# Kernel optimization log

Hardware: AMD Instinct MI355X
Metric: run time of the kernel (lower is better)

Reference implementation:

```python
import jax, jax.numpy as jnp
import numpy as np

UNITS = 1024
N_CLASSES = 41
SUBSAMPLE = 4
KERNEL = 3
FEAT = 256


def setup_inputs() -> dict:
    key = jax.random.key(0)
    ks = jax.random.split(key, 12)
    B, T, F, U, C = 32, 1000, FEAT, UNITS, N_CLASSES
    s = lambda k, shape, sc: jax.random.normal(k, shape, dtype=jnp.float32) * sc
    return {
        "x": jax.random.normal(ks[0], (B, T, F), dtype=jnp.float32),
        # depthwise conv kernel: (width, 1, channels) for WIO with groups=C
        "conv_w": s(ks[1], (KERNEL, 1, F), 0.1),
        "h0_init": s(ks[2], (1, U), 0.05),
        "w0_x": s(ks[3], (F, 3 * U), 1.0 / np.sqrt(F)),
        "w0_h": s(ks[4], (U, 3 * U), 1.0 / np.sqrt(U)),
        "b0": jnp.zeros((2, 3 * U), dtype=jnp.float32),
        "w1_x": s(ks[5], (U, 3 * U), 1.0 / np.sqrt(U)),
        "w1_h": s(ks[6], (U, 3 * U), 1.0 / np.sqrt(U)),
        "b1": jnp.zeros((2, 3 * U), dtype=jnp.float32),
        "dense_w": s(ks[7], (U, C), 1.0 / np.sqrt(U)),
        "dense_b": jnp.zeros((C,), dtype=jnp.float32),
    }


def _depthwise_conv1d(x, w):
    # x: [B, T, C], w: [K, 1, C]; SAME padding, groups = C, relu, no bias
    C = x.shape[-1]
    y = jax.lax.conv_general_dilated(
        x, w, window_strides=(1,), padding="SAME",
        dimension_numbers=("NWC", "WIO", "NWC"), feature_group_count=C)
    return jax.nn.relu(y)


def _gru_layer(x, h0, Wx, Wh, b):
    # Keras GRU v2 (reset_after=True), gate order z, r, h.
    # x: [B, T, F]; h0: [B, U]; Wx: [F, 3U]; Wh: [U, 3U]; b: [2, 3U]
    xproj = jnp.einsum("btf,fg->btg", x, Wx) + b[0]  # [B, T, 3U]
    br = b[1]

    def step(h, xp):
        rec = h @ Wh + br  # [B, 3U]
        xz, xr, xh = jnp.split(xp, 3, axis=-1)
        rz, rr, rh = jnp.split(rec, 3, axis=-1)
        z = jax.nn.sigmoid(xz + rz)
        r = jax.nn.sigmoid(xr + rr)
        hh = jnp.tanh(xh + r * rh)
        hn = z * h + (1.0 - z) * hh
        return hn, hn

    _, ys = jax.lax.scan(step, h0, jnp.swapaxes(xproj, 0, 1))  # [T, B, U]
    return jnp.swapaxes(ys, 0, 1)


def reference(x, conv_w, h0_init, w0_x, w0_h, b0, w1_x, w1_h, b1, dense_w, dense_b):
    B = x.shape[0]
    U = w0_h.shape[0]
    h = _depthwise_conv1d(x, conv_w)
    # layer 0: learned initial state tiled over batch
    h = _gru_layer(h, jnp.tile(h0_init, (B, 1)), w0_x, w0_h, b0)
    # subsample after layer nLayers-2 == 0
    h = h[:, ::SUBSAMPLE, :]
    # layer 1: zero initial state (Keras default when initial_state is None)
    h = _gru_layer(h, jnp.zeros((B, U), dtype=x.dtype), w1_x, w1_h, b1)
    return h @ dense_w + dense_b  # [B, T//4, nClasses]
```

## Files before the change

kernel.cpp:

```cpp
#include <hip/hip_runtime.h>

typedef unsigned int u32;
typedef unsigned long long u64;
typedef unsigned short u16;
typedef __attribute__((ext_vector_type(8))) short short8;
typedef __attribute__((ext_vector_type(4))) float f32x4;
typedef __attribute__((ext_vector_type(4))) unsigned int u32x4;

#define MFMA(a,b,c) __builtin_amdgcn_mfma_f32_16x16x32_bf16((a),(b),(c),0,0,0)
#define ALOAD32(p)    __hip_atomic_load((p), __ATOMIC_RELAXED, __HIP_MEMORY_SCOPE_AGENT)
#define ASTORE32(p,v) __hip_atomic_store((p),(v), __ATOMIC_RELAXED, __HIP_MEMORY_SCOPE_AGENT)

__device__ __forceinline__ float bf2f(u32 b){ union{u32 u; float f;} v; v.u = b<<16; return v.f; }
__device__ __forceinline__ u16 f2bf(float f){ union{float f; u32 u;} v; v.f = f; u32 u = v.u;
  return (u16)((u + 0x7fffu + ((u>>16)&1u)) >> 16); }
__device__ __forceinline__ u32 pack_f(float v){
  u16 hi = f2bf(v); u16 lo = f2bf(v - bf2f(hi)); return (u32)hi | ((u32)lo<<16); }

__device__ __forceinline__ void unpack8(uint4 a, uint4 b, short8& hi, short8& lo){
  u32 w[8] = {a.x,a.y,a.z,a.w,b.x,b.y,b.z,b.w};
#pragma unroll
  for (int j=0;j<8;++j){ hi[j] = (short)(w[j] & 0xffffu); lo[j] = (short)(w[j] >> 16); }
}
__device__ __forceinline__ void unpackh4(u32x4 a, short8& hi){
#pragma unroll
  for (int i=0;i<4;++i){ hi[2*i] = (short)(a[i] & 0xffffu); hi[2*i+1] = (short)(a[i] >> 16); }
}

constexpr size_t OFF_Y    = 0;
constexpr size_t OFF_SUB  = 32768000;
constexpr size_t OFF_W0XH = 65536000;
constexpr size_t OFF_W0XL = 67108864;
constexpr size_t OFF_W0HH = 68681728;
constexpr size_t OFF_W0HL = 74973184;
constexpr size_t OFF_W1XH = 81264640;
constexpr size_t OFF_W1XL = 87556096;
constexpr size_t OFF_W1HH = 93847552;
constexpr size_t OFF_W1HL = 100139008;
constexpr size_t OFF_HB0  = 106430464;
constexpr size_t OFF_HB1  = 106692608;
constexpr size_t OFF_FL0  = 106954752;
constexpr size_t OFF_FL1  = 106955776;
constexpr size_t WS_NEED  = 106956800;

__global__ void build_frags(const float* __restrict__ W, u16* __restrict__ fhi,
                            u16* __restrict__ flo, int K){
  const int KT = K >> 8;
  size_t total = (size_t)K * 12 * 256;
  for (size_t i = (size_t)blockIdx.x*blockDim.x + threadIdx.x; i < total;
       i += (size_t)gridDim.x*blockDim.x){
    int j = (int)(i & 7); size_t r = i >> 3;
    int c = (int)(r % 12); r /= 12;
    int kseg = (int)(r & 3); r >>= 2;
    int kt = (int)(r % KT); r /= KT;
    int kq = (int)(r & 7); r >>= 3;
    int wg = (int)r;
    int k = kq*(K>>3) + kt*32 + kseg*8 + j;
    int col = (c>>2)*1024 + wg*4 + (c&3);
    float v = W[(size_t)k*3072 + col];
    u16 hi = f2bf(v);
    u16 lo = f2bf(v - bf2f(hi));
    fhi[i] = hi; flo[i] = lo;
  }
}

__global__ void init_state(const float* __restrict__ h0, u32* hb0, u32* hb1,
                           int* f0, int* f1){
  int i = blockIdx.x*blockDim.x + threadIdx.x;
  if (i < 256){ f0[i]=0; f1[i]=0; }
  if (i < 16384){
    int p = i & 511;
    u32 v = (u32)f2bf(h0[2*p]) | ((u32)f2bf(h0[2*p+1]) << 16);
    hb0[i] = v;
    hb1[i] = 0u;
  }
}

__global__ void conv_pack(const float* __restrict__ x, const float* __restrict__ cw,
                          u32* __restrict__ yp){
  for (size_t i = (size_t)blockIdx.x*blockDim.x + threadIdx.x; i < 8192000ull;
       i += (size_t)gridDim.x*blockDim.x){
    int f = (int)(i & 255); int b = (int)((i>>8)&31); int t = (int)(i>>13);
    const float* xb = x + ((size_t)b*1000 + t)*256 + f;
    float acc = xb[0]*cw[256+f];
    if (t > 0)   acc += xb[-256]*cw[f];
    if (t < 999) acc += xb[256]*cw[512+f];
    acc = fmaxf(acc, 0.0f);
    yp[i] = pack_f(acc);
  }
}

template<int LAYER>
__global__ __launch_bounds__(1024, 1)
void gru_persist(const u32* __restrict__ xin,
                 const u16* __restrict__ wxf_hi, const u16* __restrict__ wxf_lo,
                 const u16* __restrict__ whf_hi, const u16* __restrict__ whf_lo,
                 const float* __restrict__ bias,
                 u32* hbuf, int* flags, u32* out_pack)
{
  constexpr int T   = (LAYER==0) ? 1000 : 250;
  constexpr int KX  = (LAYER==0) ? 256 : 1024;
  constexpr int KTX = KX >> 8;
  __shared__ u16 WxHi[8*KTX*512], WxLo[8*KTX*512];
  __shared__ u16 WhHi[8*4*512],  WhLo[8*4*512];
  __shared__ float exch[8*32*18];
  __shared__ float harr[128];
  __shared__ int hready[32];

  const int tid  = threadIdx.x;
  const int wg   = blockIdx.x;
  const int lane = tid & 63;
  const int wave = tid >> 6;
  const int m    = wave & 1;
  const int kq   = wave >> 1;
  const int u0   = wg * 4;
  const int lo16 = lane & 15, hi16 = lane >> 4;
  const int lane_off = hi16*128 + lo16*8;
  const int hsel = (kq >= 4) ? 16 : 0;

  {
    for (int i = tid; i < 8*KTX*512/4; i += 1024){ ((u64*)WxHi)[i]=0; ((u64*)WxLo)[i]=0; }
    for (int i = tid; i < 8*4*512/4;  i += 1024){ ((u64*)WhHi)[i]=0; ((u64*)WhLo)[i]=0; }
    if (tid < 32) hready[tid] = 0;
  }
  __syncthreads();
  {
    const u16* bx_hi = wxf_hi + (size_t)wg*KX*12;
    const u16* bx_lo = wxf_lo + (size_t)wg*KX*12;
    const u16* bh_hi = whf_hi + (size_t)wg*1024*12;
    const u16* bh_lo = whf_lo + (size_t)wg*1024*12;
    for (int i = tid; i < 8*KTX*48; i += 1024){
      int c = i % 12; int r = i/12; int kseg = r & 3; r >>= 2;
      int kt = r % KTX; int kqq = r / KTX;
      int ldsoff = ((kqq*KTX+kt)*4+kseg)*128 + c*8;
      *(short8*)&WxHi[ldsoff] = *(const short8*)&bx_hi[(size_t)i*8];
      *(short8*)&WxLo[ldsoff] = *(const short8*)&bx_lo[(size_t)i*8];
    }
    for (int i = tid; i < 8*4*48; i += 1024){
      int c = i % 12; int r = i/12; int kseg = r & 3; r >>= 2;
      int kt = r & 3; int kqq = r >> 2;
      int cm = (c < 8) ? c : (c + 4);
      int ldsoff = ((kqq*4+kt)*4+kseg)*128 + cm*8;
      *(short8*)&WhHi[ldsoff] = *(const short8*)&bh_hi[(size_t)i*8];
      *(short8*)&WhLo[ldsoff] = *(const short8*)&bh_lo[(size_t)i*8];
    }
    if (tid < 128){
      u16 hv = ((const u16*)hbuf)[(tid>>2)*1024 + u0 + (tid&3)];
      harr[tid] = bf2f((u32)hv);
    }
  }
  __syncthreads();

  const int eb = tid >> 2, eu_l = tid & 3, eu = u0 + eu_l;
  const float zb  = bias[eu]        + bias[3072 + eu];
  const float rbv = bias[1024 + eu] + bias[4096 + eu];
  const float hxb = bias[2048 + eu];
  const float hrb = bias[5120 + eu];

  for (int t = 0; t < T; ++t) {
    const int cur = t & 1, nxt = cur ^ 1;
    f32x4 xacc = (f32x4){0.f,0.f,0.f,0.f};
    f32x4 racc = (f32x4){0.f,0.f,0.f,0.f};
    {
      const u32* xrow = xin + ((size_t)t*32 + 16*m + lo16)*KX + kq*(KX>>3) + hi16*8;
#pragma unroll
      for (int kt = 0; kt < KTX; ++kt) {
        uint4 a0 = *(const uint4*)(xrow + kt*32);
        uint4 a1 = *(const uint4*)(xrow + kt*32 + 4);
        short8 ahi, alo; unpack8(a0, a1, ahi, alo);
        short8 bhi = *(const short8*)&WxHi[(kq*KTX+kt)*512 + lane_off];
        short8 blo = *(const short8*)&WxLo[(kq*KTX+kt)*512 + lane_off];
        xacc = MFMA(ahi, bhi, xacc);
        xacc = MFMA(alo, bhi, xacc);
        xacc = MFMA(ahi, blo, xacc);
      }
    }
    if (t > 0) {
      if (wave == 0) {
        int f0, f1;
        do { f0 = ALOAD32(flags + lane); f1 = ALOAD32(flags + 64 + lane); }
        while (!__all(f0 >= t && f1 >= t));
        asm volatile("" ::: "memory");
        if (lane == 0) ((volatile int*)hready)[0] = t;
      } else if (wave == 1) {
        int f2, f3;
        do { f2 = ALOAD32(flags + 128 + lane); f3 = ALOAD32(flags + 192 + lane); }
        while (!__all(f2 >= t && f3 >= t));
        asm volatile("" ::: "memory");
        if (lane == 0) ((volatile int*)hready)[16] = t;
      }
      while (((volatile int*)hready)[hsel] < t) { }
      asm volatile("" ::: "memory");
    }
    {
      const u32* hrow = hbuf + cur*16384 + (16*m + lo16)*512 + kq*64 + hi16*4;
      u32x4 qa, qb, qc, qd;
      asm volatile(
        "global_load_dwordx4 %0, %4, off sc0 sc1\n\t"
        "global_load_dwordx4 %1, %4, off offset:64 sc0 sc1\n\t"
        "global_load_dwordx4 %2, %4, off offset:128 sc0 sc1\n\t"
        "global_load_dwordx4 %3, %4, off offset:192 sc0 sc1\n\t"
        "s_waitcnt vmcnt(0)"
        : "=&v"(qa), "=&v"(qb), "=&v"(qc), "=&v"(qd)
        : "v"(hrow)
        : "memory");
      short8 ah0, ah1, ah2, ah3;
      unpackh4(qa, ah0); unpackh4(qb, ah1); unpackh4(qc, ah2); unpackh4(qd, ah3);
      {
        short8 bhi = *(const short8*)&WhHi[(kq*4+0)*512 + lane_off];
        short8 blo = *(const short8*)&WhLo[(kq*4+0)*512 + lane_off];
        racc = MFMA(ah0, bhi, racc); racc = MFMA(ah0, blo, racc);
      }
      {
        short8 bhi = *(const short8*)&WhHi[(kq*4+1)*512 + lane_off];
        short8 blo = *(const short8*)&WhLo[(kq*4+1)*512 + lane_off];
        racc = MFMA(ah1, bhi, racc); racc = MFMA(ah1, blo, racc);
      }
      {
        short8 bhi = *(const short8*)&WhHi[(kq*4+2)*512 + lane_off];
        short8 blo = *(const short8*)&WhLo[(kq*4+2)*512 + lane_off];
        racc = MFMA(ah2, bhi, racc); racc = MFMA(ah2, blo, racc);
      }
      {
        short8 bhi = *(const short8*)&WhHi[(kq*4+3)*512 + lane_off];
        short8 blo = *(const short8*)&WhLo[(kq*4+3)*512 + lane_off];
        racc = MFMA(ah3, bhi, racc); racc = MFMA(ah3, blo, racc);
      }
    }
    {
      const int bb = 16*m + hi16*4;
#pragma unroll
      for (int r4 = 0; r4 < 4; ++r4)
        exch[(kq*32 + bb + r4)*18 + lo16] = xacc[r4] + racc[r4];
    }
    __syncthreads();
    u32 pk_out = 0;
    if (tid < 128) {
      float zp=0.f, rp=0.f, xh=0.f, rh=0.f;
#pragma unroll
      for (int qd = 0; qd < 8; ++qd) {
        const float* e = &exch[(qd*32 + eb)*18];
        zp += e[eu_l];
        rp += e[4 + eu_l];
        xh += e[8 + eu_l];
        rh += e[12 + eu_l];
      }
      float z = 1.f/(1.f + __expf(-(zp + zb)));
      float r = 1.f/(1.f + __expf(-(rp + rbv)));
      float pre = xh + hxb + r*(rh + hrb);
      float ex = __expf(-2.f*fabsf(pre));
      float th = (1.f - ex)/(1.f + ex);
      float hh = copysignf(th, pre);
      float hn = z*harr[tid] + (1.f - z)*hh;
      harr[tid] = hn;
      pk_out = pack_f(hn);
      int pk16 = (int)(pk_out & 0xffffu);
      int prt  = __shfl_xor(pk16, 1);
      if ((tid & 1) == 0) {
        u32 pair = (u32)pk16 | ((u32)prt << 16);
        ASTORE32(hbuf + nxt*16384 + eb*512 + wg*2 + (eu_l>>1), pair);
      }
    }
    asm volatile("s_waitcnt vmcnt(0)" ::: "memory");
    __syncthreads();
    if (tid == 0)
      ASTORE32(flags + wg, t+1);
    if (tid < 128) {
      if (LAYER==0) {
        if ((t & 3) == 0)
          out_pack[((size_t)(t>>2)*32 + eb)*1024 + u0 + eu_l] = pk_out;
      } else {
        out_pack[((size_t)t*32 + eb)*1024 + u0 + eu_l] = pk_out;
      }
    }
  }
}

__global__ __launch_bounds__(256, 1)
void dense_k(const u32* __restrict__ h2, const float* __restrict__ W,
             const float* __restrict__ bias, float* __restrict__ out){
  __shared__ float rows[32*1025];
  const int ts = blockIdx.x;
  const u32* src = h2 + (size_t)ts*32768;
  for (int i = threadIdx.x; i < 32768; i += 256){
    u32 p = src[i];
    rows[(i>>10)*1025 + (i&1023)] = bf2f(p & 0xffffu) + bf2f(p >> 16);
  }
  __syncthreads();
  const int b = threadIdx.x >> 3, cg = threadIdx.x & 7;
  float acc[6] = {0.f,0.f,0.f,0.f,0.f,0.f};
  for (int k = 0; k < 1024; ++k){
    float hv = rows[b*1025 + k];
    const float* wr = W + k*41;
#pragma unroll
    for (int j = 0; j < 6; ++j){ int c = cg + 8*j; if (c < 41) acc[j] += hv*wr[c]; }
  }
#pragma unroll
  for (int j = 0; j < 6; ++j){
    int c = cg + 8*j;
    if (c < 41) out[((size_t)b*250 + ts)*41 + c] = acc[j] + bias[c];
  }
}

extern "C" void kernel_launch(void* const* d_in, const int* in_sizes, int n_in,
                              void* d_out, int out_size, void* d_ws, size_t ws_size,
                              hipStream_t stream) {
  const float* x      = (const float*)d_in[0];
  const float* conv_w = (const float*)d_in[1];
  const float* h0i    = (const float*)d_in[2];
  const float* w0x    = (const float*)d_in[3];
  const float* w0h    = (const float*)d_in[4];
  const float* b0     = (const float*)d_in[5];
  const float* w1x    = (const float*)d_in[6];
  const float* w1h    = (const float*)d_in[7];
  const float* b1     = (const float*)d_in[8];
  const float* dw     = (const float*)d_in[9];
  const float* db     = (const float*)d_in[10];
  float* outp = (float*)d_out;

  if (ws_size < WS_NEED) return;

  char* ws = (char*)d_ws;
  u32* y_pack   = (u32*)(ws + OFF_Y);
  u32* out2     = (u32*)(ws + OFF_Y);
  u32* sub_pack = (u32*)(ws + OFF_SUB);
  u16* w0x_hi = (u16*)(ws + OFF_W0XH); u16* w0x_lo = (u16*)(ws + OFF_W0XL);
  u16* w0h_hi = (u16*)(ws + OFF_W0HH); u16* w0h_lo = (u16*)(ws + OFF_W0HL);
  u16* w1x_hi = (u16*)(ws + OFF_W1XH); u16* w1x_lo = (u16*)(ws + OFF_W1XL);
  u16* w1h_hi = (u16*)(ws + OFF_W1HH); u16* w1h_lo = (u16*)(ws + OFF_W1HL);
  u32* hb0 = (u32*)(ws + OFF_HB0);
  u32* hb1 = (u32*)(ws + OFF_HB1);
  int* fl0 = (int*)(ws + OFF_FL0);
  int* fl1 = (int*)(ws + OFF_FL1);

  init_state<<<64, 512, 0, stream>>>(h0i, hb0, hb1, fl0, fl1);
  build_frags<<<2048, 256, 0, stream>>>(w0x, w0x_hi, w0x_lo, 256);
  build_frags<<<2048, 256, 0, stream>>>(w0h, w0h_hi, w0h_lo, 1024);
  build_frags<<<2048, 256, 0, stream>>>(w1x, w1x_hi, w1x_lo, 1024);
  build_frags<<<2048, 256, 0, stream>>>(w1h, w1h_hi, w1h_lo, 1024);
  conv_pack<<<4096, 256, 0, stream>>>(x, conv_w, y_pack);

  gru_persist<0><<<256, 1024, 0, stream>>>(y_pack, w0x_hi, w0x_lo, w0h_hi, w0h_lo,
                                           b0, hb0, fl0, sub_pack);
  gru_persist<1><<<256, 1024, 0, stream>>>(sub_pack, w1x_hi, w1x_lo, w1h_hi, w1h_lo,
                                           b1, hb1, fl1, out2);

  dense_k<<<250, 256, 0, stream>>>(out2, dw, db, outp);
}
```

Before: 6.468 ms.

## Split layer-0 GRU into two independent batch groups with per-group weight images

Layer 0 now runs as two groups of 128 workgroups, each owning 16 batch rows and 8 units, so each step synchronises only within its group through per-group flags. Each workgroup keeps a custom packed weight image in LDS: x and recurrent z/r/h fragments, with part of the low halves and some recurrent h weights streamed from global. A new build kernel lays out this image. The goal is lower per-step barrier and exchange latency on the serial recurrence, at the cost of more global weight reads and a complex spin-wait protocol.

```diff
diff --git a/kernel.cpp b/kernel.cpp
--- a/kernel.cpp
+++ b/kernel.cpp
@@ -29,10 +29,8 @@
 
 constexpr size_t OFF_Y    = 0;
 constexpr size_t OFF_SUB  = 32768000;
-constexpr size_t OFF_W0XH = 65536000;
-constexpr size_t OFF_W0XL = 67108864;
-constexpr size_t OFF_W0HH = 68681728;
-constexpr size_t OFF_W0HL = 74973184;
+constexpr size_t OFF_W0IH = 65536000;
+constexpr size_t OFF_W0IL = 73400320;
 constexpr size_t OFF_W1XH = 81264640;
 constexpr size_t OFF_W1XL = 87556096;
 constexpr size_t OFF_W1HH = 93847552;
@@ -64,6 +62,36 @@
   }
 }
 
+__global__ void build_w0img(const float* __restrict__ w0x, const float* __restrict__ w0h,
+                            u16* __restrict__ imgH, u16* __restrict__ imgL){
+  for (size_t i = (size_t)blockIdx.x*blockDim.x + threadIdx.x; i < 128ull*30720ull;
+       i += (size_t)gridDim.x*blockDim.x){
+    int wg = (int)(i / 30720), e = (int)(i % 30720);
+    int k, col; const float* src;
+    if (e < 4096){
+      int blk=e>>9, r=e&511, kseg=r>>7, c=(r>>3)&15, j=r&7;
+      k = blk*32 + kseg*8 + j;
+      col = (c<8) ? (wg*8+c) : (1024 + wg*8 + c-8); src = w0x;
+    } else if (e < 20480){
+      int e2=e-4096, blk=e2>>9, r=e2&511, kseg=r>>7, c=(r>>3)&15, j=r&7;
+      k = blk*32 + kseg*8 + j;
+      col = (c<8) ? (wg*8+c) : (1024 + wg*8 + c-8); src = w0h;
+    } else if (e < 24576){
+      int e2=e-20480, blk=e2>>9, r=e2&511, kseg=r>>7, c=(r>>3)&15, j=r&7;
+      k = blk*32 + kseg*8 + j;
+      if (c < 8){ col = 2048 + wg*8 + c;     src = w0x; }
+      else      { col = 2048 + wg*8 + c - 8; src = w0h; }
+    } else {
+      int e2=e-24576, blk=e2>>8, r=e2&255, kseg=r>>6, c=(r>>3)&7, j=r&7;
+      k = 256 + blk*32 + kseg*8 + j;
+      col = 2048 + wg*8 + c; src = w0h;
+    }
+    float v = src[(size_t)k*3072 + col];
+    u16 hi = f2bf(v);
+    imgH[i] = hi; imgL[i] = f2bf(v - bf2f(hi));
+  }
+}
+
 __global__ void init_state(const float* __restrict__ h0, u32* hb0, u32* hb1,
                            int* f0, int* f1){
   int i = blockIdx.x*blockDim.x + threadIdx.x;
@@ -87,6 +115,184 @@
     if (t < 999) acc += xb[256]*cw[512+f];
     acc = fmaxf(acc, 0.0f);
     yp[i] = pack_f(acc);
+  }
+}
+
+__global__ __launch_bounds__(512, 1)
+void gru8s_persist(const u32* __restrict__ xin,
+                   const u16* __restrict__ imgH, const u16* __restrict__ imgL,
+                   const float* __restrict__ bias,
+                   u32* hbuf, int* flags, u32* out_pack)
+{
+  __shared__ u16 WIMG[45056];
+  __shared__ float exch[128*33];
+  __shared__ float harr[128];
+  __shared__ int hready[32];
+
+  const int tid  = threadIdx.x;
+  const int wg   = blockIdx.x;
+  const int g    = wg >> 7;
+  const int wid  = wg & 127;
+  const int lane = tid & 63;
+  const int wave = tid >> 6;
+  const int kq   = wave;
+  const int lo16 = lane & 15, hi16 = lane >> 4;
+  const int lane_off = hi16*128 + lo16*8;
+  const int hsel = (kq >= 4) ? 16 : 0;
+
+  {
+    const u64* sH = (const u64*)(imgH + (size_t)wid*30720);
+    const u64* sL = (const u64*)(imgL + (size_t)wid*30720 + 4096);
+    u64* dH = (u64*)WIMG;
+    u64* dL = (u64*)(WIMG + 24576);
+    for (int i = tid; i < 6144; i += 512) dH[i] = sH[i];
+    for (int i = tid; i < 5120; i += 512) dL[i] = sL[i];
+    if (tid < 32) hready[tid] = 0;
+    if (tid < 128){
+      u16 hv = ((const u16*)hbuf)[g*16384 + (tid>>3)*1024 + wid*8 + (tid&7)];
+      harr[tid] = bf2f((u32)hv);
+    }
+  }
+  __syncthreads();
+
+  const u16* zrx_h  = &WIMG[kq*512 + lane_off];
+  const u16* zrxg_l = imgL + (size_t)wid*30720 + kq*512 + lane_off;
+  const u16* zrh_h  = &WIMG[4096 + kq*2048 + lane_off];
+  const u16* hhx_h  = &WIMG[20480 + kq*512 + lane_off];
+  const bool hhLds  = (kq < 2);
+  const u16* hhb_h; const u16* hhb_l; int hhstride;
+  if (hhLds){
+    hhb_h = &WIMG[20480 + kq*2048 + lane_off]; hhb_l = hhb_h + 20480; hhstride = 512;
+  } else {
+    size_t go = (size_t)wid*30720 + 24576 + (size_t)(kq-2)*1024 + hi16*64
+              + ((lo16 >= 8) ? (lo16-8)*8 : 0);
+    hhb_h = imgH + go; hhb_l = imgL + go; hhstride = 256;
+  }
+
+  const int gs = tid >> 3, gu = tid & 7, eu = wid*8 + gu;
+  const float zb  = bias[eu]        + bias[3072 + eu];
+  const float rbv = bias[1024 + eu] + bias[4096 + eu];
+  const float hxb = bias[2048 + eu];
+  const float hrb = bias[5120 + eu];
+
+  for (int t = 0; t < 1000; ++t) {
+    const int cur = t & 1, nxt = cur ^ 1;
+    f32x4 aZR = (f32x4){0.f,0.f,0.f,0.f};
+    f32x4 aHX = (f32x4){0.f,0.f,0.f,0.f};
+    f32x4 aHR = (f32x4){0.f,0.f,0.f,0.f};
+    {
+      const u32* xr = xin + ((size_t)t*32 + g*16 + lo16)*256 + kq*32 + hi16*8;
+      uint4 a0 = *(const uint4*)xr;
+      uint4 a1 = *(const uint4*)(xr + 4);
+      short8 ahi, alo; unpack8(a0, a1, ahi, alo);
+      short8 b1h = *(const short8*)zrx_h, b1l = *(const short8*)zrxg_l;
+      short8 b2h = *(const short8*)hhx_h, b2l = *(const short8*)(hhx_h + 20480);
+      aZR = MFMA(ahi,b1h,aZR); aZR = MFMA(alo,b1h,aZR); aZR = MFMA(ahi,b1l,aZR);
+      aHX = MFMA(ahi,b2h,aHX); aHX = MFMA(alo,b2h,aHX); aHX = MFMA(ahi,b2l,aHX);
+    }
+    if (t > 0) {
+      if (wave == 0) {
+        int f0;
+        do { f0 = ALOAD32(flags + g*128 + lane); } while (__all(f0 >= t) == 0);
+        asm volatile("" ::: "memory");
+        if (lane == 0) ((volatile int*)hready)[0] = t;
+      } else if (wave == 1) {
+        int f1;
+        do { f1 = ALOAD32(flags + g*128 + 64 + lane); } while (__all(f1 >= t) == 0);
+        asm volatile("" ::: "memory");
+        if (lane == 0) ((volatile int*)hready)[16] = t;
+      }
+      while (((volatile int*)hready)[hsel] < t) { }
+      asm volatile("" ::: "memory");
+    }
+    {
+      const u32* hrow = hbuf + cur*16384 + g*8192 + lo16*512 + kq*64 + hi16*4;
+      u32x4 qa, qb, qc, qd;
+      asm volatile(
+        "global_load_dwordx4 %0, %4, off sc0 sc1\n\t"
+        "global_load_dwordx4 %1, %4, off offset:64 sc0 sc1\n\t"
+        "global_load_dwordx4 %2, %4, off offset:128 sc0 sc1\n\t"
+        "global_load_dwordx4 %3, %4, off offset:192 sc0 sc1\n\t"
+        "s_waitcnt vmcnt(0)"
+        : "=&v"(qa), "=&v"(qb), "=&v"(qc), "=&v"(qd)
+        : "v"(hrow)
+        : "memory");
+      short8 ah0, ah1, ah2, ah3;
+      unpackh4(qa, ah0); unpackh4(qb, ah1); unpackh4(qc, ah2); unpackh4(qd, ah3);
+      {
+        short8 b1h = *(const short8*)(zrh_h + 0*512);
+        short8 b1l = *(const short8*)(zrh_h + 0*512 + 20480);
+        short8 b2h = *(const short8*)(hhb_h + 0*hhstride);
+        short8 b2l = *(const short8*)(hhb_l + 0*hhstride);
+        aZR = MFMA(ah0,b1h,aZR); aZR = MFMA(ah0,b1l,aZR);
+        aHR = MFMA(ah0,b2h,aHR); aHR = MFMA(ah0,b2l,aHR);
+      }
+      {
+        short8 b1h = *(const short8*)(zrh_h + 1*512);
+        short8 b1l = *(const short8*)(zrh_h + 1*512 + 20480);
+        short8 b2h = *(const short8*)(hhb_h + 1*hhstride);
+        short8 b2l = *(const short8*)(hhb_l + 1*hhstride);
+        aZR = MFMA(ah1,b1h,aZR); aZR = MFMA(ah1,b1l,aZR);
+        aHR = MFMA(ah1,b2h,aHR); aHR = MFMA(ah1,b2l,aHR);
+      }
+      {
+        short8 b1h = *(const short8*)(zrh_h + 2*512);
+        short8 b1l = *(const short8*)(zrh_h + 2*512 + 20480);
+        short8 b2h = *(const short8*)(hhb_h + 2*hhstride);
+        short8 b2l = *(const short8*)(hhb_l + 2*hhstride);
+        aZR = MFMA(ah2,b1h,aZR); aZR = MFMA(ah2,b1l,aZR);
+        aHR = MFMA(ah2,b2h,aHR); aHR = MFMA(ah2,b2l,aHR);
+      }
+      {
+        short8 b1h = *(const short8*)(zrh_h + 3*512);
+        short8 b1l = *(const short8*)(zrh_h + 3*512 + 20480);
+        short8 b2h = *(const short8*)(hhb_h + 3*hhstride);
+        short8 b2l = *(const short8*)(hhb_l + 3*hhstride);
+        aZR = MFMA(ah3,b1h,aZR); aZR = MFMA(ah3,b1l,aZR);
+        aHR = MFMA(ah3,b2h,aHR); aHR = MFMA(ah3,b2l,aHR);
+      }
+    }
+    {
+      const int bb = hi16*4;
+#pragma unroll
+      for (int r4 = 0; r4 < 4; ++r4){
+        exch[(kq*16 + bb + r4)*33 + lo16]      = aZR[r4];
+        exch[(kq*16 + bb + r4)*33 + 16 + lo16] = (lo16 < 8) ? aHX[r4] : aHR[r4];
+      }
+    }
+    __syncthreads();
+    u32 pk_out = 0;
+    if (tid < 128) {
+      float zp=0.f, rp=0.f, xh=0.f, rh=0.f;
+#pragma unroll
+      for (int k8 = 0; k8 < 8; ++k8){
+        const float* e = &exch[(k8*16 + gs)*33];
+        zp += e[gu]; rp += e[8+gu]; xh += e[16+gu]; rh += e[24+gu];
+      }
+      float z = 1.f/(1.f + __expf(-(zp + zb)));
+      float r = 1.f/(1.f + __expf(-(rp + rbv)));
+      float pre = xh + hxb + r*(rh + hrb);
+      float ex = __expf(-2.f*fabsf(pre));
+      float th = (1.f - ex)/(1.f + ex);
+      float hh = copysignf(th, pre);
+      float hn = z*harr[tid] + (1.f - z)*hh;
+      harr[tid] = hn;
+      pk_out = pack_f(hn);
+      int pk16 = (int)(pk_out & 0xffffu);
+      int prt  = __shfl_xor(pk16, 1);
+      if ((tid & 1) == 0) {
+        u32 pair = (u32)pk16 | ((u32)prt << 16);
+        ASTORE32(hbuf + nxt*16384 + g*8192 + gs*512 + wid*4 + (gu>>1), pair);
+      }
+    }
+    asm volatile("s_waitcnt vmcnt(0)" ::: "memory");
+    __syncthreads();
+    if (tid == 0)
+      ASTORE32(flags + g*128 + wid, t+1);
+    if (tid < 128) {
+      if ((t & 3) == 0)
+        out_pack[((size_t)(t>>2)*32 + g*16 + gs)*1024 + eu] = pk_out;
+    }
   }
 }
 
@@ -324,8 +530,7 @@
   u32* y_pack   = (u32*)(ws + OFF_Y);
   u32* out2     = (u32*)(ws + OFF_Y);
   u32* sub_pack = (u32*)(ws + OFF_SUB);
-  u16* w0x_hi = (u16*)(ws + OFF_W0XH); u16* w0x_lo = (u16*)(ws + OFF_W0XL);
-  u16* w0h_hi = (u16*)(ws + OFF_W0HH); u16* w0h_lo = (u16*)(ws + OFF_W0HL);
+  u16* w0iH = (u16*)(ws + OFF_W0IH); u16* w0iL = (u16*)(ws + OFF_W0IL);
   u16* w1x_hi = (u16*)(ws + OFF_W1XH); u16* w1x_lo = (u16*)(ws + OFF_W1XL);
   u16* w1h_hi = (u16*)(ws + OFF_W1HH); u16* w1h_lo = (u16*)(ws + OFF_W1HL);
   u32* hb0 = (u32*)(ws + OFF_HB0);
@@ -334,14 +539,12 @@
   int* fl1 = (int*)(ws + OFF_FL1);
 
   init_state<<<64, 512, 0, stream>>>(h0i, hb0, hb1, fl0, fl1);
-  build_frags<<<2048, 256, 0, stream>>>(w0x, w0x_hi, w0x_lo, 256);
-  build_frags<<<2048, 256, 0, stream>>>(w0h, w0h_hi, w0h_lo, 1024);
+  build_w0img<<<2048, 256, 0, stream>>>(w0x, w0h, w0iH, w0iL);
   build_frags<<<2048, 256, 0, stream>>>(w1x, w1x_hi, w1x_lo, 1024);
   build_frags<<<2048, 256, 0, stream>>>(w1h, w1h_hi, w1h_lo, 1024);
   conv_pack<<<4096, 256, 0, stream>>>(x, conv_w, y_pack);
 
-  gru_persist<0><<<256, 1024, 0, stream>>>(y_pack, w0x_hi, w0x_lo, w0h_hi, w0h_lo,
-                                           b0, hb0, fl0, sub_pack);
+  gru8s_persist<<<256, 512, 0, stream>>>(y_pack, w0iH, w0iL, b0, hb0, fl0, sub_pack);
   gru_persist<1><<<256, 1024, 0, stream>>>(sub_pack, w1x_hi, w1x_lo, w1h_hi, w1h_lo,
                                            b1, hb1, fl1, out2);
 
```

After: 5.990 ms. -7.4%, faster.
